# Optimization experiments

Measured on AMD Instinct MI355X. Metric: run time of the kernel, lower is better.

## Reference

```python
import jax, jax.numpy as jnp
import numpy as np

T, D = 2048, 2048
H, H_KV, DH = 32, 8, 64
I = 5632
EPS = 1e-5


def setup_inputs() -> dict:
    key = jax.random.key(0)
    ks = jax.random.split(key, 9)
    s = 0.02
    return {
        "x": jax.random.normal(ks[0], (T, D), dtype=jnp.float32),
        "ln1_w": jnp.ones((D,), dtype=jnp.float32),
        "ln2_w": jnp.ones((D,), dtype=jnp.float32),
        "wq": jax.random.normal(ks[1], (D, H * DH), dtype=jnp.float32) * s,
        "wk": jax.random.normal(ks[2], (D, H_KV * DH), dtype=jnp.float32) * s,
        "wv": jax.random.normal(ks[3], (D, H_KV * DH), dtype=jnp.float32) * s,
        "wo": jax.random.normal(ks[4], (H * DH, D), dtype=jnp.float32) * s,
        "w1": jax.random.normal(ks[5], (D, 2 * I), dtype=jnp.float32) * s,
        "w2": jax.random.normal(ks[6], (I, D), dtype=jnp.float32) * s,
    }


def _rmsnorm(x, w):
    var = jnp.mean(x * x, axis=-1, keepdims=True)
    return x * jax.lax.rsqrt(var + EPS) * w


def reference(x, ln1_w, ln2_w, wq, wk, wv, wo, w1, w2):
    t, d = x.shape
    h = _rmsnorm(x, ln1_w)
    # projections -> (heads, T, head_dim)
    q = (h @ wq).reshape(t, H, DH).transpose(1, 0, 2)
    k = (h @ wk).reshape(t, H_KV, DH).transpose(1, 0, 2)
    v = (h @ wv).reshape(t, H_KV, DH).transpose(1, 0, 2)
    # GQA: query head hq uses kv head hq * H_KV // H == hq // (H // H_KV)
    rep = H // H_KV
    k = jnp.repeat(k, rep, axis=0)  # (H, T, DH)
    v = jnp.repeat(v, rep, axis=0)
    scale = 1.0 / np.sqrt(DH)
    scores = jnp.einsum('htd,hsd->hts', q, k) * scale  # (H, T, T)
    causal = jnp.tril(jnp.ones((t, t), dtype=bool))
    neg = jnp.asarray(jnp.finfo(scores.dtype).min, scores.dtype)
    scores = jnp.where(causal[None, :, :], scores, neg)
    weights = jax.nn.softmax(scores, axis=-1)
    attn = jnp.einsum('hts,hsd->htd', weights, v)  # (H, T, DH)
    attn = attn.transpose(1, 0, 2).reshape(t, H * DH)
    x = x + attn @ wo
    h2 = _rmsnorm(x, ln2_w)
    fc1 = h2 @ w1  # (T, 2I)
    gate, val = fc1[:, :I], fc1[:, I:]
    sw = jax.nn.silu(gate) * val
    return x + sw @ w2
```

## Files before the change

### kernel.cpp

```cpp
#include <hip/hip_runtime.h>
#include <hip/hip_bf16.h>
#include <cstdint>
#include <cstddef>

#define TT 2048
#define DD 2048
#define NHQ 32
#define NHKV 8
#define DHD 64
#define II 5632

typedef short short8 __attribute__((ext_vector_type(8)));
typedef __bf16 bf16x8 __attribute__((ext_vector_type(8)));
typedef float f32x4 __attribute__((ext_vector_type(4)));

__device__ __forceinline__ float b2f(unsigned short u) {
  union { float f; unsigned int i; } v; v.i = ((unsigned int)u) << 16; return v.f;
}
__device__ __forceinline__ unsigned short f2b(float f) {
  union { float f; unsigned int i; } v; v.f = f;
  unsigned int r = v.i + 0x7FFFu + ((v.i >> 16) & 1u);
  return (unsigned short)(r >> 16);
}

__device__ __forceinline__ void gload16(const unsigned short* g, unsigned short* l) {
  __builtin_amdgcn_global_load_lds(
      (const __attribute__((address_space(1))) void*)g,
      (__attribute__((address_space(3))) void*)(unsigned int)(uintptr_t)l,
      16, 0, 0);
}

__global__ void transpose_f32_bf16(const float* __restrict__ src,
                                   unsigned short* __restrict__ dst,
                                   int K, int N) {
  __shared__ float tile[32][33];
  const int bn = blockIdx.x * 32;
  const int bk = blockIdx.y * 32;
  const int tx = threadIdx.x, ty = threadIdx.y;
#pragma unroll
  for (int i = 0; i < 32; i += 8)
    tile[ty + i][tx] = src[(size_t)(bk + ty + i) * N + bn + tx];
  __syncthreads();
#pragma unroll
  for (int i = 0; i < 32; i += 8)
    dst[(size_t)(bn + ty + i) * K + bk + tx] = f2b(tile[tx][ty + i]);
}

__global__ void rmsnorm_kernel(const float* __restrict__ x,
                               const float* __restrict__ w,
                               unsigned short* __restrict__ out) {
  const int row = blockIdx.x;
  const float* xr = x + (size_t)row * DD;
  const int t = threadIdx.x;
  float4 v0 = ((const float4*)xr)[t];
  float4 v1 = ((const float4*)xr)[t + 256];
  float ss = v0.x * v0.x + v0.y * v0.y + v0.z * v0.z + v0.w * v0.w +
             v1.x * v1.x + v1.y * v1.y + v1.z * v1.z + v1.w * v1.w;
#pragma unroll
  for (int off = 32; off >= 1; off >>= 1) ss += __shfl_xor(ss, off);
  __shared__ float sred[4];
  if ((t & 63) == 0) sred[t >> 6] = ss;
  __syncthreads();
  float tot = sred[0] + sred[1] + sred[2] + sred[3];
  float rs = rsqrtf(tot * (1.0f / DD) + 1e-5f);
  float4 w0 = ((const float4*)w)[t];
  float4 w1v = ((const float4*)w)[t + 256];
  unsigned short* orow = out + (size_t)row * DD;
  ushort4 o0, o1;
  o0.x = f2b(v0.x * rs * w0.x); o0.y = f2b(v0.y * rs * w0.y);
  o0.z = f2b(v0.z * rs * w0.z); o0.w = f2b(v0.w * rs * w0.w);
  o1.x = f2b(v1.x * rs * w1v.x); o1.y = f2b(v1.y * rs * w1v.y);
  o1.z = f2b(v1.z * rs * w1v.z); o1.w = f2b(v1.w * rs * w1v.w);
  ((ushort4*)orow)[t] = o0;
  ((ushort4*)orow)[t + 256] = o1;
}

template <int EPI>
__global__ void gemm_bt(const unsigned short* __restrict__ A, int lda,
                        const unsigned short* __restrict__ Bt, int ldb,
                        int K,
                        const float* __restrict__ resid,
                        void* __restrict__ Cout, int ldc) {
  __shared__ __align__(16) unsigned short As[128 * 32];
  __shared__ __align__(16) unsigned short Bs[128 * 32];
  const int bm = blockIdx.y * 128;
  const int bn = blockIdx.x * 128;
  const int tid = threadIdx.x;
  const int lane = tid & 63;
  const int L = lane & 15, G = lane >> 4;
  const int w = tid >> 6;
  const int wr = (w >> 1) * 64, wc = (w & 1) * 64;

  const f32x4 zero = {0.f, 0.f, 0.f, 0.f};
  f32x4 acc[4][4];
#pragma unroll
  for (int m = 0; m < 4; ++m)
#pragma unroll
    for (int n = 0; n < 4; ++n) acc[m][n] = zero;

  const int srow = w * 32 + (lane >> 2);
  const int scol = (lane & 3) * 8;
  const unsigned short* gA = A + (size_t)(bm + srow) * lda + scol;
  const unsigned short* gB = Bt + (size_t)(bn + srow) * ldb + scol;
  unsigned short* lA0 = &As[w * 1024];
  unsigned short* lA1 = &As[w * 1024 + 512];
  unsigned short* lB0 = &Bs[w * 1024];
  unsigned short* lB1 = &Bs[w * 1024 + 512];

  const int nk = K >> 5;
  for (int kt = 0; kt < nk; ++kt) {
    const int ko = kt * 32;
    __syncthreads();
    gload16(gA + ko, lA0);
    gload16(gA + (size_t)16 * lda + ko, lA1);
    gload16(gB + ko, lB0);
    gload16(gB + (size_t)16 * ldb + ko, lB1);
    __syncthreads();
    bf16x8 af[4], bfr[4];
#pragma unroll
    for (int m = 0; m < 4; ++m)
      af[m] = *reinterpret_cast<const bf16x8*>(&As[(wr + m * 16 + L) * 32 + G * 8]);
#pragma unroll
    for (int n = 0; n < 4; ++n)
      bfr[n] = *reinterpret_cast<const bf16x8*>(&Bs[(wc + n * 16 + L) * 32 + G * 8]);
#pragma unroll
    for (int m = 0; m < 4; ++m)
#pragma unroll
      for (int n = 0; n < 4; ++n)
        acc[m][n] = __builtin_amdgcn_mfma_f32_16x16x32_bf16(af[m], bfr[n], acc[m][n], 0, 0, 0);
  }

#pragma unroll
  for (int m = 0; m < 4; ++m)
#pragma unroll
    for (int n = 0; n < 4; ++n)
#pragma unroll
      for (int i = 0; i < 4; ++i) {
        const int r = bm + wr + m * 16 + G * 4 + i;
        const int c = bn + wc + n * 16 + L;
        const float val = acc[m][n][i];
        if constexpr (EPI == 0) {
          ((unsigned short*)Cout)[(size_t)r * ldc + c] = f2b(val);
        } else {
          ((float*)Cout)[(size_t)r * ldc + c] = val + resid[(size_t)r * ldc + c];
        }
      }
}

__launch_bounds__(256, 2)
__global__ void attn_kernel(const unsigned short* __restrict__ qkv,
                            unsigned short* __restrict__ out) {
  const int hq = blockIdx.x;
  const int qb = blockIdx.y;
  const int hkv = hq >> 2;
  const int tid = threadIdx.x, lane = tid & 63, w = tid >> 6;
  const int L = lane & 15, G = lane >> 4;

  __shared__ __align__(16) unsigned short Ks[64 * 72];
  __shared__ __align__(16) unsigned short Vt[64 * 72];
  __shared__ __align__(16) unsigned short Ps[4][16 * 72];

  const int qrow = qb * 64 + w * 16;
  bf16x8 qf[2];
#pragma unroll
  for (int d0 = 0; d0 < 2; ++d0)
    qf[d0] = *reinterpret_cast<const bf16x8*>(
        qkv + (size_t)(qrow + L) * 3072 + hq * 64 + d0 * 32 + G * 8);

  const f32x4 zero = {0.f, 0.f, 0.f, 0.f};
  f32x4 o[4];
#pragma unroll
  for (int n = 0; n < 4; ++n) o[n] = zero;
  float mrow[4], lrow[4];
#pragma unroll
  for (int i = 0; i < 4; ++i) { mrow[i] = -1e30f; lrow[i] = 0.f; }

  const int ntile = qb + 1;
  for (int t = 0; t < ntile; ++t) {
    const int s0 = t * 64;
    __syncthreads();
#pragma unroll
    for (int i2 = 0; i2 < 2; ++i2) {
      const int c = i2 * 256 + tid;
      const int r = c >> 3, col = (c & 7) * 8;
      bf16x8 k8 = *reinterpret_cast<const bf16x8*>(
          qkv + (size_t)(s0 + r) * 3072 + 2048 + hkv * 64 + col);
      *reinterpret_cast<bf16x8*>(&Ks[r * 72 + col]) = k8;
      short8 v8 = *reinterpret_cast<const short8*>(
          qkv + (size_t)(s0 + r) * 3072 + 2560 + hkv * 64 + col);
#pragma unroll
      for (int j = 0; j < 8; ++j) {
        const int d = col + j;
        Vt[d * 72 + (r ^ (((d >> 3) & 7) << 3))] = (unsigned short)v8[j];
      }
    }
    __syncthreads();

    f32x4 sacc[4];
#pragma unroll
    for (int nt = 0; nt < 4; ++nt) {
      sacc[nt] = zero;
#pragma unroll
      for (int d0 = 0; d0 < 2; ++d0) {
        bf16x8 kf = *reinterpret_cast<const bf16x8*>(
            &Ks[(nt * 16 + L) * 72 + d0 * 32 + G * 8]);
        sacc[nt] = __builtin_amdgcn_mfma_f32_16x16x32_bf16(qf[d0], kf, sacc[nt], 0, 0, 0);
      }
    }

    float pt[4][4];
#pragma unroll
    for (int i = 0; i < 4; ++i) {
      const int q = qrow + G * 4 + i;
      float mx = mrow[i];
#pragma unroll
      for (int nt = 0; nt < 4; ++nt) {
        float sv = sacc[nt][i] * 0.125f;
        const int s = s0 + nt * 16 + L;
        sv = (s <= q) ? sv : -1e30f;
        pt[i][nt] = sv;
        mx = fmaxf(mx, sv);
      }
#pragma unroll
      for (int off = 1; off < 16; off <<= 1) mx = fmaxf(mx, __shfl_xor(mx, off));
      const float scale_o = __expf(mrow[i] - mx);
      float rsum = 0.f;
#pragma unroll
      for (int nt = 0; nt < 4; ++nt) {
        const float p = __expf(pt[i][nt] - mx);
        pt[i][nt] = p;
        rsum += p;
      }
#pragma unroll
      for (int off = 1; off < 16; off <<= 1) rsum += __shfl_xor(rsum, off);
      mrow[i] = mx;
      lrow[i] = lrow[i] * scale_o + rsum;
#pragma unroll
      for (int nt = 0; nt < 4; ++nt) o[nt][i] *= scale_o;
    }

#pragma unroll
    for (int i = 0; i < 4; ++i) {
      const int prow = G * 4 + i;
#pragma unroll
      for (int nt = 0; nt < 4; ++nt)
        Ps[w][prow * 72 + ((nt * 16 + L) ^ ((prow & 7) << 3))] = f2b(pt[i][nt]);
    }
#pragma unroll
    for (int kc = 0; kc < 2; ++kc) {
      bf16x8 pf = *reinterpret_cast<const bf16x8*>(
          &Ps[w][L * 72 + ((kc * 32 + G * 8) ^ ((L & 7) << 3))]);
#pragma unroll
      for (int nt = 0; nt < 4; ++nt) {
        const int vrow = nt * 16 + L;
        bf16x8 vf = *reinterpret_cast<const bf16x8*>(
            &Vt[vrow * 72 + ((kc * 32 + G * 8) ^ (((vrow >> 3) & 7) << 3))]);
        o[nt] = __builtin_amdgcn_mfma_f32_16x16x32_bf16(pf, vf, o[nt], 0, 0, 0);
      }
    }
  }

#pragma unroll
  for (int nt = 0; nt < 4; ++nt)
#pragma unroll
    for (int i = 0; i < 4; ++i) {
      const float val = o[nt][i] / lrow[i];
      out[(size_t)(qrow + G * 4 + i) * 2048 + hq * 64 + nt * 16 + L] = f2b(val);
    }
}

__global__ void swiglu_kernel(unsigned short* __restrict__ fc1) {
  const size_t total = (size_t)TT * (II / 8);
  const size_t idx = (size_t)blockIdx.x * blockDim.x + threadIdx.x;
  if (idx >= total) return;
  const int m = (int)(idx / (II / 8));
  const int jc = (int)(idx % (II / 8));
  unsigned short* g = fc1 + (size_t)m * (2 * II) + jc * 8;
  short8 gv = *(const short8*)g;
  short8 vv = *(const short8*)(g + II);
  short8 ov;
#pragma unroll
  for (int j = 0; j < 8; ++j) {
    const float gf = b2f((unsigned short)gv[j]);
    const float vf = b2f((unsigned short)vv[j]);
    const float s = gf / (1.f + __expf(-gf));
    ov[j] = (short)f2b(s * vf);
  }
  *(short8*)g = ov;
}

extern "C" void kernel_launch(void* const* d_in, const int* in_sizes, int n_in,
                              void* d_out, int out_size, void* d_ws, size_t ws_size,
                              hipStream_t stream) {
  const float* x    = (const float*)d_in[0];
  const float* ln1w = (const float*)d_in[1];
  const float* ln2w = (const float*)d_in[2];
  const float* wq   = (const float*)d_in[3];
  const float* wk   = (const float*)d_in[4];
  const float* wv   = (const float*)d_in[5];
  const float* wo   = (const float*)d_in[6];
  const float* w1   = (const float*)d_in[7];
  const float* w2   = (const float*)d_in[8];
  float* outp = (float*)d_out;

  char* ws = (char*)d_ws;
  size_t off = 0;
  auto alloc = [&](size_t bytes) {
    char* p = ws + off;
    off += (bytes + 255) & ~(size_t)255;
    return p;
  };
  unsigned short* wqkvT = (unsigned short*)alloc((size_t)3072 * 2048 * 2);
  unsigned short* woT   = (unsigned short*)alloc((size_t)2048 * 2048 * 2);
  unsigned short* w1T   = (unsigned short*)alloc((size_t)11264 * 2048 * 2);
  unsigned short* w2T   = (unsigned short*)alloc((size_t)2048 * 5632 * 2);
  unsigned short* h     = (unsigned short*)alloc((size_t)2048 * 2048 * 2);
  unsigned short* qkv   = (unsigned short*)alloc((size_t)2048 * 3072 * 2);
  unsigned short* attnb = (unsigned short*)alloc((size_t)2048 * 2048 * 2);
  float*          x2    = (float*)alloc((size_t)2048 * 2048 * 4);
  unsigned short* h2    = (unsigned short*)alloc((size_t)2048 * 2048 * 2);
  unsigned short* fc1   = (unsigned short*)alloc((size_t)2048 * 11264 * 2);
  (void)ws_size; (void)in_sizes; (void)n_in; (void)out_size;

  dim3 tb(32, 8);
  transpose_f32_bf16<<<dim3(2048 / 32, 2048 / 32), tb, 0, stream>>>(wq, wqkvT, 2048, 2048);
  transpose_f32_bf16<<<dim3(512 / 32, 2048 / 32), tb, 0, stream>>>(wk, wqkvT + (size_t)2048 * 2048, 2048, 512);
  transpose_f32_bf16<<<dim3(512 / 32, 2048 / 32), tb, 0, stream>>>(wv, wqkvT + (size_t)2560 * 2048, 2048, 512);
  transpose_f32_bf16<<<dim3(2048 / 32, 2048 / 32), tb, 0, stream>>>(wo, woT, 2048, 2048);
  transpose_f32_bf16<<<dim3(11264 / 32, 2048 / 32), tb, 0, stream>>>(w1, w1T, 2048, 11264);
  transpose_f32_bf16<<<dim3(2048 / 32, 5632 / 32), tb, 0, stream>>>(w2, w2T, 5632, 2048);

  rmsnorm_kernel<<<2048, 256, 0, stream>>>(x, ln1w, h);

  gemm_bt<0><<<dim3(3072 / 128, 2048 / 128), 256, 0, stream>>>(
      h, 2048, wqkvT, 2048, 2048, nullptr, qkv, 3072);

  attn_kernel<<<dim3(NHQ, TT / 64), 256, 0, stream>>>(qkv, attnb);

  gemm_bt<1><<<dim3(2048 / 128, 2048 / 128), 256, 0, stream>>>(
      attnb, 2048, woT, 2048, 2048, x, x2, 2048);

  rmsnorm_kernel<<<2048, 256, 0, stream>>>(x2, ln2w, h2);

  gemm_bt<0><<<dim3(11264 / 128, 2048 / 128), 256, 0, stream>>>(
      h2, 2048, w1T, 2048, 2048, nullptr, fc1, 11264);

  swiglu_kernel<<<5632, 256, 0, stream>>>(fc1);

  gemm_bt<1><<<dim3(2048 / 128, 2048 / 128), 256, 0, stream>>>(
      fc1, 11264, w2T, 5632, 5632, x2, outp, 2048);
}
```

Measured before the change: 679.6 us.

## Add wide 128x256 GEMM for FC1, vectorize weight transpose, skip causal mask off-diagonal

Adds a 512-thread GEMM with 128x256 tiles and a 4-stage global-to-LDS pipeline, used for the large FC1 projection, to raise operand reuse and hide load latency. The weight transpose now converts to bf16 before storing into LDS and uses 64x64 tiles with float4 loads and ushort4 stores, cutting memory transactions. In attention, the causal mask comparison runs only on the diagonal block. The new GEMM uses more LDS and threads per block, which may limit occupancy.

New measurement: 670.0 us. Within noise of the previous version (-1.4%).

```diff
diff --git a/kernel.cpp b/kernel.cpp
--- a/kernel.cpp
+++ b/kernel.cpp
@@ -30,20 +30,37 @@
       16, 0, 0);
 }
 
+#define WAITVM(N) asm volatile("s_waitcnt vmcnt(" #N ")" ::: "memory")
+#define BARRIER() do { asm volatile("" ::: "memory"); __builtin_amdgcn_s_barrier(); \
+                       asm volatile("" ::: "memory"); } while (0)
+
 __global__ void transpose_f32_bf16(const float* __restrict__ src,
                                    unsigned short* __restrict__ dst,
                                    int K, int N) {
-  __shared__ float tile[32][33];
-  const int bn = blockIdx.x * 32;
-  const int bk = blockIdx.y * 32;
-  const int tx = threadIdx.x, ty = threadIdx.y;
-#pragma unroll
-  for (int i = 0; i < 32; i += 8)
-    tile[ty + i][tx] = src[(size_t)(bk + ty + i) * N + bn + tx];
+  __shared__ unsigned short tile[64][70];
+  const int bn = blockIdx.x * 64;
+  const int bk = blockIdx.y * 64;
+  const int tid = threadIdx.x;
+  const int rr = tid >> 4, c4 = (tid & 15) * 4;
+#pragma unroll
+  for (int j = 0; j < 4; ++j) {
+    const int r = rr + j * 16;
+    float4 v = *(const float4*)(src + (size_t)(bk + r) * N + bn + c4);
+    ushort4 u;
+    u.x = f2b(v.x); u.y = f2b(v.y); u.z = f2b(v.z); u.w = f2b(v.w);
+    *(ushort4*)&tile[r][c4] = u;
+  }
   __syncthreads();
 #pragma unroll
-  for (int i = 0; i < 32; i += 8)
-    dst[(size_t)(bn + ty + i) * K + bk + tx] = f2b(tile[tx][ty + i]);
+  for (int j = 0; j < 4; ++j) {
+    const int n = rr + j * 16;
+    ushort4 u;
+    u.x = tile[c4 + 0][n];
+    u.y = tile[c4 + 1][n];
+    u.z = tile[c4 + 2][n];
+    u.w = tile[c4 + 3][n];
+    *(ushort4*)(dst + (size_t)(bn + n) * K + bk + c4) = u;
+  }
 }
 
 __global__ void rmsnorm_kernel(const float* __restrict__ x,
@@ -147,6 +164,105 @@
       }
 }
 
+template <int EPI>
+__launch_bounds__(512, 2)
+__global__ void gemm_bt_wide(const unsigned short* __restrict__ A, int lda,
+                             const unsigned short* __restrict__ Bt, int ldb,
+                             int K,
+                             const float* __restrict__ resid,
+                             void* __restrict__ Cout, int ldc) {
+  __shared__ __align__(16) unsigned short As[4][128 * 32];
+  __shared__ __align__(16) unsigned short Bs[4][256 * 32];
+  const int bm = blockIdx.y * 128;
+  const int bn = blockIdx.x * 256;
+  const int tid = threadIdx.x;
+  const int lane = tid & 63;
+  const int L = lane & 15, G = lane >> 4;
+  const int w = tid >> 6;
+  const int wr = (w >> 2) * 64;
+  const int wc = (w & 3) * 64;
+
+  const f32x4 zero = {0.f, 0.f, 0.f, 0.f};
+  f32x4 acc[4][4];
+#pragma unroll
+  for (int m = 0; m < 4; ++m)
+#pragma unroll
+    for (int n = 0; n < 4; ++n) acc[m][n] = zero;
+
+  const int arow = tid >> 2;
+  const int slot = (tid & 3) * 8;
+  const unsigned short* gA = A + (size_t)(bm + arow) * lda + slot;
+  const unsigned short* gB0 = Bt + (size_t)(bn + arow) * ldb + slot;
+  const unsigned short* gB1 = Bt + (size_t)(bn + 128 + arow) * ldb + slot;
+  const int ldsA = w * 512;
+  const int ldsB0 = w * 512;
+  const int ldsB1 = 4096 + w * 512;
+
+  const int nk = K >> 5;
+
+  gload16(gA, &As[0][ldsA]);
+  gload16(gB0, &Bs[0][ldsB0]);
+  gload16(gB1, &Bs[0][ldsB1]);
+  gload16(gA + 32, &As[1][ldsA]);
+  gload16(gB0 + 32, &Bs[1][ldsB0]);
+  gload16(gB1 + 32, &Bs[1][ldsB1]);
+
+  int cb = 0;
+  int ko = 64;
+
+  auto COMPUTE = [&](int b) {
+    bf16x8 af[4], bfr[4];
+#pragma unroll
+    for (int m = 0; m < 4; ++m)
+      af[m] = *reinterpret_cast<const bf16x8*>(&As[b][(wr + m * 16 + L) * 32 + G * 8]);
+#pragma unroll
+    for (int n = 0; n < 4; ++n)
+      bfr[n] = *reinterpret_cast<const bf16x8*>(&Bs[b][(wc + n * 16 + L) * 32 + G * 8]);
+    __builtin_amdgcn_s_setprio(1);
+#pragma unroll
+    for (int m = 0; m < 4; ++m)
+#pragma unroll
+      for (int n = 0; n < 4; ++n)
+        acc[m][n] = __builtin_amdgcn_mfma_f32_16x16x32_bf16(af[m], bfr[n], acc[m][n], 0, 0, 0);
+    __builtin_amdgcn_s_setprio(0);
+  };
+
+  for (int t = 0; t < nk - 2; ++t) {
+    const int sb = (cb + 2) & 3;
+    gload16(gA + ko, &As[sb][ldsA]);
+    gload16(gB0 + ko, &Bs[sb][ldsB0]);
+    gload16(gB1 + ko, &Bs[sb][ldsB1]);
+    ko += 32;
+    WAITVM(6);
+    BARRIER();
+    COMPUTE(cb);
+    cb = (cb + 1) & 3;
+  }
+  WAITVM(3);
+  BARRIER();
+  COMPUTE(cb);
+  cb = (cb + 1) & 3;
+  WAITVM(0);
+  BARRIER();
+  COMPUTE(cb);
+
+#pragma unroll
+  for (int m = 0; m < 4; ++m)
+#pragma unroll
+    for (int n = 0; n < 4; ++n)
+#pragma unroll
+      for (int i = 0; i < 4; ++i) {
+        const int r = bm + wr + m * 16 + G * 4 + i;
+        const int c = bn + wc + n * 16 + L;
+        const float val = acc[m][n][i];
+        if constexpr (EPI == 0) {
+          ((unsigned short*)Cout)[(size_t)r * ldc + c] = f2b(val);
+        } else {
+          ((float*)Cout)[(size_t)r * ldc + c] = val + resid[(size_t)r * ldc + c];
+        }
+      }
+}
+
 __launch_bounds__(256, 2)
 __global__ void attn_kernel(const unsigned short* __restrict__ qkv,
                             unsigned short* __restrict__ out) {
@@ -208,6 +324,7 @@
       }
     }
 
+    const bool diag = (t == qb);
     float pt[4][4];
 #pragma unroll
     for (int i = 0; i < 4; ++i) {
@@ -216,8 +333,10 @@
 #pragma unroll
       for (int nt = 0; nt < 4; ++nt) {
         float sv = sacc[nt][i] * 0.125f;
-        const int s = s0 + nt * 16 + L;
-        sv = (s <= q) ? sv : -1e30f;
+        if (diag) {
+          const int s = s0 + nt * 16 + L;
+          sv = (s <= q) ? sv : -1e30f;
+        }
         pt[i][nt] = sv;
         mx = fmaxf(mx, sv);
       }
@@ -322,13 +441,12 @@
   unsigned short* fc1   = (unsigned short*)alloc((size_t)2048 * 11264 * 2);
   (void)ws_size; (void)in_sizes; (void)n_in; (void)out_size;
 
-  dim3 tb(32, 8);
-  transpose_f32_bf16<<<dim3(2048 / 32, 2048 / 32), tb, 0, stream>>>(wq, wqkvT, 2048, 2048);
-  transpose_f32_bf16<<<dim3(512 / 32, 2048 / 32), tb, 0, stream>>>(wk, wqkvT + (size_t)2048 * 2048, 2048, 512);
-  transpose_f32_bf16<<<dim3(512 / 32, 2048 / 32), tb, 0, stream>>>(wv, wqkvT + (size_t)2560 * 2048, 2048, 512);
-  transpose_f32_bf16<<<dim3(2048 / 32, 2048 / 32), tb, 0, stream>>>(wo, woT, 2048, 2048);
-  transpose_f32_bf16<<<dim3(11264 / 32, 2048 / 32), tb, 0, stream>>>(w1, w1T, 2048, 11264);
-  transpose_f32_bf16<<<dim3(2048 / 32, 5632 / 32), tb, 0, stream>>>(w2, w2T, 5632, 2048);
+  transpose_f32_bf16<<<dim3(2048 / 64, 2048 / 64), 256, 0, stream>>>(wq, wqkvT, 2048, 2048);
+  transpose_f32_bf16<<<dim3(512 / 64, 2048 / 64), 256, 0, stream>>>(wk, wqkvT + (size_t)2048 * 2048, 2048, 512);
+  transpose_f32_bf16<<<dim3(512 / 64, 2048 / 64), 256, 0, stream>>>(wv, wqkvT + (size_t)2560 * 2048, 2048, 512);
+  transpose_f32_bf16<<<dim3(2048 / 64, 2048 / 64), 256, 0, stream>>>(wo, woT, 2048, 2048);
+  transpose_f32_bf16<<<dim3(11264 / 64, 2048 / 64), 256, 0, stream>>>(w1, w1T, 2048, 11264);
+  transpose_f32_bf16<<<dim3(2048 / 64, 5632 / 64), 256, 0, stream>>>(w2, w2T, 5632, 2048);
 
   rmsnorm_kernel<<<2048, 256, 0, stream>>>(x, ln1w, h);
 
@@ -342,7 +460,7 @@
 
   rmsnorm_kernel<<<2048, 256, 0, stream>>>(x2, ln2w, h2);
 
-  gemm_bt<0><<<dim3(11264 / 128, 2048 / 128), 256, 0, stream>>>(
+  gemm_bt_wide<0><<<dim3(11264 / 256, 2048 / 128), 512, 0, stream>>>(
       h2, 2048, w1T, 2048, 2048, nullptr, fc1, 11264);
 
   swiglu_kernel<<<5632, 256, 0, stream>>>(fc1);
```
